# Kernel optimization log

Hardware: AMD Instinct MI355X
Metric: run time of the kernel (lower is better)

The kernel has to match this reference:

```python
import jax, jax.numpy as jnp
import numpy as np


def _dsconv(x, dw_w, dw_b, pw_w, pw_b):
    # depthwise 3x3 (padding=1, stride=1) + pointwise 1x1, both with bias (PyTorch Conv2d default)
    C = x.shape[1]
    y = jax.lax.conv_general_dilated(
        x, dw_w, window_strides=(1, 1), padding=((1, 1), (1, 1)),
        dimension_numbers=('NCHW', 'OIHW', 'NCHW'), feature_group_count=C)
    y = y + dw_b[None, :, None, None]
    y = jnp.einsum('bchw,oc->bohw', y, pw_w) + pw_b[None, :, None, None]
    return y


def setup_inputs() -> dict:
    key = jax.random.key(0)
    ks = jax.random.split(key, 16)
    B, C, H, W = 8, 256, 64, 256
    inp = {"x": jax.random.normal(ks[0], (B, C, H, W), dtype=jnp.float32)}
    chans = [(C, 128), (128, 64), (64, 32), (32, 9)]
    ki = 1
    for li, (ci, co) in enumerate(chans, start=1):
        inp[f"dw{li}_w"] = jax.random.normal(ks[ki], (ci, 1, 3, 3), dtype=jnp.float32) / 3.0; ki += 1
        inp[f"dw{li}_b"] = jnp.zeros((ci,), dtype=jnp.float32)
        inp[f"pw{li}_w"] = jax.random.normal(ks[ki], (co, ci), dtype=jnp.float32) / jnp.sqrt(jnp.float32(ci)); ki += 1
        inp[f"pw{li}_b"] = jnp.zeros((co,), dtype=jnp.float32)
    return inp


def reference(x,
              dw1_w, dw1_b, pw1_w, pw1_b,
              dw2_w, dw2_b, pw2_w, pw2_b,
              dw3_w, dw3_b, pw3_w, pw3_b,
              dw4_w, dw4_b, pw4_w, pw4_b):
    # la_conv stack: DSConv->ReLU x3, final DSConv (no relu), out channels = 9
    a = jax.nn.relu(_dsconv(x, dw1_w, dw1_b, pw1_w, pw1_b))
    a = jax.nn.relu(_dsconv(a, dw2_w, dw2_b, pw2_w, pw2_b))
    a = jax.nn.relu(_dsconv(a, dw3_w, dw3_b, pw3_w, pw3_b))
    a = _dsconv(a, dw4_w, dw4_b, pw4_w, pw4_b)            # (B,9,H,W)
    attn = jax.nn.softmax(a, axis=1)                      # softmax over the 9 taps

    B, C, H, W = x.shape
    xpad = jnp.pad(x, ((0, 0), (0, 0), (1, 1), (1, 1)))
    # dynamic 3x3 conv: out[b,c,i,j] = sum_{ki,kj} xpad[b,c,i+ki,j+kj] * attn[b,ki*3+kj,i,j]
    out = jnp.zeros_like(x)
    for ki in range(3):
        for kj in range(3):
            out = out + xpad[:, :, ki:ki + H, kj:kj + W] * attn[:, ki * 3 + kj][:, None, :, :]

    char_attn = attn.transpose(0, 2, 3, 1).reshape(B, H, W, 3, 3)
    return out, char_attn
```

## Files before the change

kernel.cpp:

```cpp
#include <hip/hip_runtime.h>
#include <math.h>

#define BH_ 64
#define BW_ 256
constexpr size_t HW = (size_t)BH_ * BW_;

using f32x4   = __attribute__((ext_vector_type(4))) float;
using short8  = __attribute__((ext_vector_type(8))) short;
using short4v = __attribute__((ext_vector_type(4))) short;

__device__ __forceinline__ short f2bf(float f) {
    unsigned u = __float_as_uint(f);
    u += 0x7fffu + ((u >> 16) & 1u);
    return (short)(u >> 16);
}
__device__ __forceinline__ float bf2f(short s) {
    return __uint_as_float(((unsigned)(unsigned short)s) << 16);
}

__device__ __forceinline__ int xcd_swizzle() {
    const int rb  = blockIdx.x;
    const int cpx = gridDim.x >> 3;
    return (rb & 7) * cpx + (rb >> 3);
}

__global__ __launch_bounds__(256)
void prep_kernel(const float* __restrict__ p1,
                 const float* __restrict__ p2,
                 const float* __restrict__ p3,
                 short* __restrict__ wb1,
                 short* __restrict__ wb2,
                 float* __restrict__ wt3)
{
    int idx = blockIdx.x * 256 + threadIdx.x;
    if (idx < 128 * 256) {
        wb1[idx] = f2bf(p1[idx]);
    } else if (idx < 128 * 256 + 64 * 128) {
        int r = idx - 128 * 256;
        wb2[r] = f2bf(p2[r]);
    } else if (idx < 128 * 256 + 64 * 128 + 32 * 64) {
        int r = idx - (128 * 256 + 64 * 128);
        int ci = r / 32, co = r % 32;
        wt3[r] = p3[co * 64 + ci];
    }
}

template<int CI, int CO, bool INBF>
__global__ __launch_bounds__(256, 4)
void dsconv_mfma(const void* __restrict__ xin_,
                 const float* __restrict__ dww,
                 const float* __restrict__ dwb,
                 const short* __restrict__ wBf,
                 const float* __restrict__ pwb,
                 short* __restrict__ out)
{
    constexpr int CIC = 32;
    constexpr int PX  = 64;
    constexpr int NT  = CO / 16;
    constexpr int WNT = NT / 4;
    constexpr int ST  = 40;
    constexpr int NC  = CI / CIC;
    static_assert(NT % 4 == 0 && CI % CIC == 0, "geometry");

    __shared__ short Abuf[2][PX * ST];

    const int t    = threadIdx.x;
    const int w    = t >> 6;
    const int lane = t & 63;
    const int bid  = xcd_swizzle();
    const int jt   = bid & 3;
    const int i    = (bid >> 2) & 63;
    const int b    = bid >> 8;
    const int j0   = jt * PX;

    const int ci_l = t >> 3;
    const int g    = t & 7;
    const int jq   = j0 + g * 8;
    const bool vtop = (i > 0), vbot = (i < BH_ - 1);

    const int lm = lane & 15;
    const int kb = lane >> 4;

    f32x4 acc[4][WNT];
    #pragma unroll
    for (int q = 0; q < WNT; ++q) {
        float bv = pwb[(w * WNT + q) * 16 + lm];
        #pragma unroll
        for (int mt = 0; mt < 4; ++mt) {
            f32x4 z = {bv, bv, bv, bv};
            acc[mt][q] = z;
        }
    }

    float  xw[3][10];
    float  wv9[9];
    float  dwbv;
    short8 bcur[WNT], bnxt[WNT];

    const short* bbase[WNT];
    #pragma unroll
    for (int q = 0; q < WNT; ++q)
        bbase[q] = wBf + (size_t)((w * WNT + q) * 16 + lm) * CI + kb * 8;

    auto LOADBF = [&](int cc, short8* dst) {
        #pragma unroll
        for (int q = 0; q < WNT; ++q)
            dst[q] = *reinterpret_cast<const short8*>(bbase[q] + cc);
    };

    auto LOADX = [&](int cc) {
        const int ci = cc + ci_l;
        #pragma unroll
        for (int di = 0; di < 3; ++di) {
            const bool ok = (di == 0) ? vtop : (di == 2) ? vbot : true;
            if (ok) {
                if constexpr (INBF) {
                    const short* xp = (const short*)xin_ + ((size_t)b * CI + ci) * HW;
                    const short* xr = xp + (size_t)(i + di - 1) * BW_ + jq;
                    xw[di][0] = (jq > 0) ? bf2f(xr[-1]) : 0.f;
                    short8 S = *reinterpret_cast<const short8*>(xr);
                    #pragma unroll
                    for (int e = 0; e < 8; ++e) xw[di][1 + e] = bf2f(S[e]);
                    xw[di][9] = (jq + 8 < BW_) ? bf2f(xr[8]) : 0.f;
                } else {
                    const float* xp = (const float*)xin_ + ((size_t)b * CI + ci) * HW;
                    const float* xr = xp + (size_t)(i + di - 1) * BW_ + jq;
                    xw[di][0] = (jq > 0) ? xr[-1] : 0.f;
                    float4 A = *reinterpret_cast<const float4*>(xr);
                    float4 Bq = *reinterpret_cast<const float4*>(xr + 4);
                    xw[di][1] = A.x; xw[di][2] = A.y; xw[di][3] = A.z; xw[di][4] = A.w;
                    xw[di][5] = Bq.x; xw[di][6] = Bq.y; xw[di][7] = Bq.z; xw[di][8] = Bq.w;
                    xw[di][9] = (jq + 8 < BW_) ? xr[8] : 0.f;
                }
            } else {
                #pragma unroll
                for (int e = 0; e < 10; ++e) xw[di][e] = 0.f;
            }
        }
        const float* wkp = dww + ci * 9;
        #pragma unroll
        for (int k = 0; k < 9; ++k) wv9[k] = wkp[k];
        dwbv = dwb[ci];
    };

    auto STOREA = [&](int nb) {
        float o[8];
        #pragma unroll
        for (int e = 0; e < 8; ++e) o[e] = dwbv;
        #pragma unroll
        for (int di = 0; di < 3; ++di) {
            const float w0 = wv9[di * 3 + 0];
            const float w1 = wv9[di * 3 + 1];
            const float w2 = wv9[di * 3 + 2];
            #pragma unroll
            for (int e = 0; e < 8; ++e)
                o[e] += w0 * xw[di][e] + w1 * xw[di][e + 1] + w2 * xw[di][e + 2];
        }
        #pragma unroll
        for (int e = 0; e < 8; ++e) {
            int px = g * 8 + e;
            int sa = (px * ST + ci_l) ^ (((px >> 3) & 7) << 3);
            Abuf[nb][sa] = f2bf(o[e]);
        }
    };

    auto MFMASTEP = [&](int nb) {
        #pragma unroll
        for (int mt = 0; mt < 4; ++mt) {
            int px = mt * 16 + lm;
            int sa = (px * ST + kb * 8) ^ (((px >> 3) & 7) << 3);
            short8 af = *reinterpret_cast<const short8*>(&Abuf[nb][sa]);
            #pragma unroll
            for (int q = 0; q < WNT; ++q)
                acc[mt][q] = __builtin_amdgcn_mfma_f32_16x16x32_bf16(
                    af, bcur[q], acc[mt][q], 0, 0, 0);
        }
    };

    LOADX(0); LOADBF(0, bcur);
    STOREA(0);
    __syncthreads();

    for (int c = 0; c < NC; ++c) {
        if (c + 1 < NC) { LOADX((c + 1) * CIC); LOADBF((c + 1) * CIC, bnxt); }
        MFMASTEP(c & 1);
        if (c + 1 < NC) {
            STOREA((c + 1) & 1);
            #pragma unroll
            for (int q = 0; q < WNT; ++q) bcur[q] = bnxt[q];
            __syncthreads();
        }
    }

    #pragma unroll
    for (int mt = 0; mt < 4; ++mt) {
        #pragma unroll
        for (int q = 0; q < WNT; ++q) {
            int co = (w * WNT + q) * 16 + lm;
            short* op = out + (((size_t)b * CO + co) * BH_ + i) * BW_
                        + j0 + mt * 16 + kb * 4;
            short4v v;
            v[0] = f2bf(fmaxf(acc[mt][q][0], 0.f));
            v[1] = f2bf(fmaxf(acc[mt][q][1], 0.f));
            v[2] = f2bf(fmaxf(acc[mt][q][2], 0.f));
            v[3] = f2bf(fmaxf(acc[mt][q][3], 0.f));
            *reinterpret_cast<short4v*>(op) = v;
        }
    }
}

template<int CI, int CO, int CPT>
__global__ __launch_bounds__(256, 4)
void dsconv_kernel(const short* __restrict__ xin,
                   const float* __restrict__ dww,
                   const float* __restrict__ dwb,
                   const float* __restrict__ wT,
                   const float* __restrict__ pwb,
                   short* __restrict__ out)
{
    constexpr int CIC = 32;
    constexpr int PX  = 64;
    static_assert(CO / CPT == 16, "co groups must be 16");

    __shared__ float dwbuf[CIC * PX];
    __shared__ float wbuf[CIC * CO];

    const int t   = threadIdx.x;
    const int bid = xcd_swizzle();
    const int jt  = bid & 3;
    const int i   = (bid >> 2) & 63;
    const int b   = bid >> 8;
    const int j0  = jt * PX;

    const int px_g = t & 15;
    const int co_g = t >> 4;
    const int co0  = co_g * CPT;
    const int p0   = px_g * 4;

    const int ci_local = t >> 3;
    const int g        = t & 7;
    const int jq       = j0 + g * 8;

    float acc[CPT][4];
    #pragma unroll
    for (int ii = 0; ii < CPT; ++ii) {
        float bv = pwb[co0 + ii];
        #pragma unroll
        for (int jj = 0; jj < 4; ++jj) acc[ii][jj] = bv;
    }

    for (int cc = 0; cc < CI; cc += CIC) {
        __syncthreads();
        {
            const float* src = wT + (size_t)cc * CO;
            #pragma unroll
            for (int idx = t * 4; idx < CIC * CO; idx += 1024)
                *reinterpret_cast<float4*>(&wbuf[idx]) =
                    *reinterpret_cast<const float4*>(&src[idx]);
        }
        {
            const int ci = cc + ci_local;
            const float* wk = dww + ci * 9;
            float w[9];
            #pragma unroll
            for (int k = 0; k < 9; ++k) w[k] = wk[k];
            float o[8];
            float bv = dwb[ci];
            #pragma unroll
            for (int e = 0; e < 8; ++e) o[e] = bv;

            const short* xp = xin + ((size_t)b * CI + ci) * HW;
            #pragma unroll
            for (int di = -1; di <= 1; ++di) {
                int ii2 = i + di;
                if ((unsigned)ii2 < (unsigned)BH_) {
                    const short* xr = xp + (size_t)ii2 * BW_ + jq;
                    float v[10];
                    v[0] = (jq > 0) ? bf2f(xr[-1]) : 0.f;
                    short8 S = *reinterpret_cast<const short8*>(xr);
                    #pragma unroll
                    for (int e = 0; e < 8; ++e) v[1 + e] = bf2f(S[e]);
                    v[9] = (jq + 8 < BW_) ? bf2f(xr[8]) : 0.f;
                    const float w0 = w[(di + 1) * 3 + 0];
                    const float w1 = w[(di + 1) * 3 + 1];
                    const float w2 = w[(di + 1) * 3 + 2];
                    #pragma unroll
                    for (int e = 0; e < 8; ++e)
                        o[e] += w0 * v[e] + w1 * v[e + 1] + w2 * v[e + 2];
                }
            }
            float4* dst = reinterpret_cast<float4*>(&dwbuf[ci_local * PX + g * 8]);
            dst[0] = make_float4(o[0], o[1], o[2], o[3]);
            dst[1] = make_float4(o[4], o[5], o[6], o[7]);
        }
        __syncthreads();

        #pragma unroll 4
        for (int k = 0; k < CIC; ++k) {
            float4 dq = *reinterpret_cast<const float4*>(&dwbuf[k * PX + p0]);
            float dv[4] = {dq.x, dq.y, dq.z, dq.w};
            float wv2[CPT];
            if constexpr (CPT == 2) {
                float2 wq = *reinterpret_cast<const float2*>(&wbuf[k * CO + co0]);
                wv2[0] = wq.x; wv2[1] = wq.y;
            } else {
                float4 wq = *reinterpret_cast<const float4*>(&wbuf[k * CO + co0]);
                #pragma unroll
                for (int ii = 0; ii < CPT && ii < 4; ++ii) wv2[ii] = (&wq.x)[ii];
            }
            #pragma unroll
            for (int ii = 0; ii < CPT; ++ii)
                #pragma unroll
                for (int jj = 0; jj < 4; ++jj)
                    acc[ii][jj] += wv2[ii] * dv[jj];
        }
    }

    #pragma unroll
    for (int ii = 0; ii < CPT; ++ii) {
        short4v v;
        v[0] = f2bf(fmaxf(acc[ii][0], 0.f));
        v[1] = f2bf(fmaxf(acc[ii][1], 0.f));
        v[2] = f2bf(fmaxf(acc[ii][2], 0.f));
        v[3] = f2bf(fmaxf(acc[ii][3], 0.f));
        short* op = out + (((size_t)b * CO + co0 + ii) * BH_ + i) * BW_ + j0 + p0;
        *reinterpret_cast<short4v*>(op) = v;
    }
}

__global__ __launch_bounds__(256, 4)
void final_kernel(const float* __restrict__ x,
                  const short* __restrict__ a3,
                  const float* __restrict__ dww,
                  const float* __restrict__ dwb,
                  const float* __restrict__ pww,
                  const float* __restrict__ pwb,
                  float* __restrict__ out,
                  float* __restrict__ chat)
{
    constexpr int PX = 64;
    __shared__ float dwbuf[32 * PX];
    __shared__ float attL[9][PX];

    const int t   = threadIdx.x;
    const int bid = xcd_swizzle();
    const int jt  = bid & 3;
    const int i   = (bid >> 2) & 63;
    const int b   = bid >> 8;
    const int j0  = jt * PX;
    const int g   = t & 7;
    const int jq  = j0 + g * 8;

    {
        const int ci = t >> 3;
        const float* wk = dww + ci * 9;
        float w[9];
        #pragma unroll
        for (int k = 0; k < 9; ++k) w[k] = wk[k];
        float o[8];
        float bv = dwb[ci];
        #pragma unroll
        for (int e = 0; e < 8; ++e) o[e] = bv;

        const short* xp = a3 + ((size_t)b * 32 + ci) * HW;
        #pragma unroll
        for (int di = -1; di <= 1; ++di) {
            int ii2 = i + di;
            if ((unsigned)ii2 < (unsigned)BH_) {
                const short* xr = xp + (size_t)ii2 * BW_ + jq;
                float v[10];
                v[0] = (jq > 0) ? bf2f(xr[-1]) : 0.f;
                short8 S = *reinterpret_cast<const short8*>(xr);
                #pragma unroll
                for (int e = 0; e < 8; ++e) v[1 + e] = bf2f(S[e]);
                v[9] = (jq + 8 < BW_) ? bf2f(xr[8]) : 0.f;
                const float w0 = w[(di + 1) * 3 + 0];
                const float w1 = w[(di + 1) * 3 + 1];
                const float w2 = w[(di + 1) * 3 + 2];
                #pragma unroll
                for (int e = 0; e < 8; ++e)
                    o[e] += w0 * v[e] + w1 * v[e + 1] + w2 * v[e + 2];
            }
        }
        float4* dst = reinterpret_cast<float4*>(&dwbuf[(t >> 3) * PX + g * 8]);
        dst[0] = make_float4(o[0], o[1], o[2], o[3]);
        dst[1] = make_float4(o[4], o[5], o[6], o[7]);
    }
    __syncthreads();

    for (int idx = t; idx < 9 * PX; idx += 256) {
        int co = idx >> 6;
        int px = idx & 63;
        float acc = pwb[co];
        #pragma unroll
        for (int ci = 0; ci < 32; ++ci)
            acc += pww[co * 32 + ci] * dwbuf[ci * PX + px];
        attL[co][px] = acc;
    }
    __syncthreads();

    if (t < PX) {
        float v[9];
        float m = -1e30f;
        #pragma unroll
        for (int k = 0; k < 9; ++k) { v[k] = attL[k][t]; m = fmaxf(m, v[k]); }
        float s = 0.f;
        #pragma unroll
        for (int k = 0; k < 9; ++k) { v[k] = __expf(v[k] - m); s += v[k]; }
        float inv = 1.f / s;
        #pragma unroll
        for (int k = 0; k < 9; ++k) attL[k][t] = v[k] * inv;
    }
    __syncthreads();

    {
        size_t base = (((size_t)b * BH_ + i) * BW_ + j0) * 9;
        for (int idx = t; idx < PX * 9; idx += 256)
            chat[base + idx] = attL[idx % 9][idx / 9];
    }

    float ar[9][8];
    #pragma unroll
    for (int k = 0; k < 9; ++k) {
        float4 a0 = *reinterpret_cast<const float4*>(&attL[k][g * 8]);
        float4 a1 = *reinterpret_cast<const float4*>(&attL[k][g * 8 + 4]);
        ar[k][0] = a0.x; ar[k][1] = a0.y; ar[k][2] = a0.z; ar[k][3] = a0.w;
        ar[k][4] = a1.x; ar[k][5] = a1.y; ar[k][6] = a1.z; ar[k][7] = a1.w;
    }

    const int c0 = t >> 3;
    for (int c = c0; c < 256; c += 32) {
        const float* xp = x + ((size_t)b * 256 + c) * HW;
        float v3[3][10];
        #pragma unroll
        for (int di = 0; di < 3; ++di) {
            int ii2 = i + di - 1;
            if ((unsigned)ii2 < (unsigned)BH_) {
                const float* xr = xp + (size_t)ii2 * BW_ + jq;
                v3[di][0] = (jq > 0) ? xr[-1] : 0.f;
                float4 A = *reinterpret_cast<const float4*>(xr);
                float4 Bq = *reinterpret_cast<const float4*>(xr + 4);
                v3[di][1] = A.x; v3[di][2] = A.y; v3[di][3] = A.z; v3[di][4] = A.w;
                v3[di][5] = Bq.x; v3[di][6] = Bq.y; v3[di][7] = Bq.z; v3[di][8] = Bq.w;
                v3[di][9] = (jq + 8 < BW_) ? xr[8] : 0.f;
            } else {
                #pragma unroll
                for (int e = 0; e < 10; ++e) v3[di][e] = 0.f;
            }
        }
        float o[8];
        #pragma unroll
        for (int e = 0; e < 8; ++e) o[e] = 0.f;
        #pragma unroll
        for (int di = 0; di < 3; ++di)
            #pragma unroll
            for (int dj = 0; dj < 3; ++dj)
                #pragma unroll
                for (int e = 0; e < 8; ++e)
                    o[e] += v3[di][e + dj] * ar[di * 3 + dj][e];
        float* op = out + ((size_t)b * 256 + c) * HW + (size_t)i * BW_ + jq;
        *reinterpret_cast<float4*>(op)     = make_float4(o[0], o[1], o[2], o[3]);
        *reinterpret_cast<float4*>(op + 4) = make_float4(o[4], o[5], o[6], o[7]);
    }
}

extern "C" void kernel_launch(void* const* d_in, const int* in_sizes, int n_in,
                              void* d_out, int out_size, void* d_ws, size_t ws_size,
                              hipStream_t stream)
{
    const float* x    = (const float*)d_in[0];
    const float* dw1w = (const float*)d_in[1];
    const float* dw1b = (const float*)d_in[2];
    const float* pw1w = (const float*)d_in[3];
    const float* pw1b = (const float*)d_in[4];
    const float* dw2w = (const float*)d_in[5];
    const float* dw2b = (const float*)d_in[6];
    const float* pw2w = (const float*)d_in[7];
    const float* pw2b = (const float*)d_in[8];
    const float* dw3w = (const float*)d_in[9];
    const float* dw3b = (const float*)d_in[10];
    const float* pw3w = (const float*)d_in[11];
    const float* pw3b = (const float*)d_in[12];
    const float* dw4w = (const float*)d_in[13];
    const float* dw4b = (const float*)d_in[14];
    const float* pw4w = (const float*)d_in[15];
    const float* pw4b = (const float*)d_in[16];

    float* outp = (float*)d_out;
    float* chat = outp + (size_t)8 * 256 * HW;

    short* wb1 = (short*)d_ws;
    short* wb2 = wb1 + 128 * 256;
    float* wt3 = (float*)((char*)d_ws + 81920);
    short* abase = (short*)((char*)d_ws + 90112);

    int kmax = 1;
    for (int k = 8; k >= 1; k >>= 1) {
        size_t need = 90112 + (size_t)k * (128 + 64) * HW * sizeof(short);
        if (need <= ws_size) { kmax = k; break; }
    }
    short* a1 = abase;
    short* a2 = a1 + (size_t)kmax * 128 * HW;
    short* a3 = a1;

    prep_kernel<<<(128 * 256 + 64 * 128 + 32 * 64 + 255) / 256, 256, 0, stream>>>(
        pw1w, pw2w, pw3w, wb1, wb2, wt3);

    for (int b0 = 0; b0 < 8; b0 += kmax) {
        int kc = (8 - b0 < kmax) ? (8 - b0) : kmax;
        const float* xb = x + (size_t)b0 * 256 * HW;
        int grid64 = kc * 256;

        dsconv_mfma<256, 128, false><<<grid64, 256, 0, stream>>>(
            xb, dw1w, dw1b, wb1, pw1b, a1);
        dsconv_mfma<128, 64, true><<<grid64, 256, 0, stream>>>(
            a1, dw2w, dw2b, wb2, pw2b, a2);
        dsconv_kernel<64, 32, 2><<<grid64, 256, 0, stream>>>(
            a2, dw3w, dw3b, wt3, pw3b, a3);
        final_kernel<<<grid64, 256, 0, stream>>>(
            xb, a3, dw4w, dw4b, pw4w, pw4b,
            outp + (size_t)b0 * 256 * HW, chat + (size_t)b0 * HW * 9);
    }
}
```

Before: 222.4 us.

## Stage full depthwise output in LDS once, then run MFMA loop without barriers

The double-buffered chunked pipeline is replaced by two phases. First every channel chunk's depthwise 3x3 result is computed and written into a single LDS tile holding all CI channels, followed by one barrier. Then the pointwise MFMA loop reads from that tile with no per-chunk __syncthreads. This removes a barrier per chunk and lets the compiler unroll freely, but LDS per block grows (for CI=256, about 33KB), which may cut occupancy, and depthwise global loads no longer overlap MFMA work.

```diff
diff --git a/kernel.cpp b/kernel.cpp
--- a/kernel.cpp
+++ b/kernel.cpp
@@ -58,11 +58,11 @@
     constexpr int PX  = 64;
     constexpr int NT  = CO / 16;
     constexpr int WNT = NT / 4;
-    constexpr int ST  = 40;
+    constexpr int ST  = CI + 8;
     constexpr int NC  = CI / CIC;
     static_assert(NT % 4 == 0 && CI % CIC == 0, "geometry");
 
-    __shared__ short Abuf[2][PX * ST];
+    __shared__ short Abuf[PX * ST];
 
     const int t    = threadIdx.x;
     const int w    = t >> 6;
@@ -81,6 +81,69 @@
     const int lm = lane & 15;
     const int kb = lane >> 4;
 
+    {
+        const int aswz = ((jq >> 3) & 7) << 3;
+        #pragma unroll
+        for (int c = 0; c < NC; ++c) {
+            const int cc = c * CIC;
+            const int ci = cc + ci_l;
+
+            float xw[3][10];
+            #pragma unroll
+            for (int di = 0; di < 3; ++di) {
+                const bool ok = (di == 0) ? vtop : (di == 2) ? vbot : true;
+                if (ok) {
+                    if constexpr (INBF) {
+                        const short* xp = (const short*)xin_ + ((size_t)b * CI + ci) * HW;
+                        const short* xr = xp + (size_t)(i + di - 1) * BW_ + jq;
+                        xw[di][0] = (jq > 0) ? bf2f(xr[-1]) : 0.f;
+                        short8 S = *reinterpret_cast<const short8*>(xr);
+                        #pragma unroll
+                        for (int e = 0; e < 8; ++e) xw[di][1 + e] = bf2f(S[e]);
+                        xw[di][9] = (jq + 8 < BW_) ? bf2f(xr[8]) : 0.f;
+                    } else {
+                        const float* xp = (const float*)xin_ + ((size_t)b * CI + ci) * HW;
+                        const float* xr = xp + (size_t)(i + di - 1) * BW_ + jq;
+                        xw[di][0] = (jq > 0) ? xr[-1] : 0.f;
+                        float4 A = *reinterpret_cast<const float4*>(xr);
+                        float4 Bq = *reinterpret_cast<const float4*>(xr + 4);
+                        xw[di][1] = A.x; xw[di][2] = A.y; xw[di][3] = A.z; xw[di][4] = A.w;
+                        xw[di][5] = Bq.x; xw[di][6] = Bq.y; xw[di][7] = Bq.z; xw[di][8] = Bq.w;
+                        xw[di][9] = (jq + 8 < BW_) ? xr[8] : 0.f;
+                    }
+                } else {
+                    #pragma unroll
+                    for (int e = 0; e < 10; ++e) xw[di][e] = 0.f;
+                }
+            }
+
+            const float* wkp = dww + ci * 9;
+            float o[8];
+            {
+                const float dwbv = dwb[ci];
+                #pragma unroll
+                for (int e = 0; e < 8; ++e) o[e] = dwbv;
+            }
+            #pragma unroll
+            for (int di = 0; di < 3; ++di) {
+                const float w0 = wkp[di * 3 + 0];
+                const float w1 = wkp[di * 3 + 1];
+                const float w2 = wkp[di * 3 + 2];
+                #pragma unroll
+                for (int e = 0; e < 8; ++e)
+                    o[e] += w0 * xw[di][e] + w1 * xw[di][e + 1] + w2 * xw[di][e + 2];
+            }
+            #pragma unroll
+            for (int e = 0; e < 8; ++e) {
+                int px = g * 8 + e;
+                int sa = (px * ST + ci) ^ aswz;
+                Abuf[sa] = f2bf(o[e]);
+            }
+        }
+    }
+
+    __syncthreads();
+
     f32x4 acc[4][WNT];
     #pragma unroll
     for (int q = 0; q < WNT; ++q) {
@@ -92,104 +155,35 @@
         }
     }
 
-    float  xw[3][10];
-    float  wv9[9];
-    float  dwbv;
-    short8 bcur[WNT], bnxt[WNT];
-
     const short* bbase[WNT];
     #pragma unroll
     for (int q = 0; q < WNT; ++q)
         bbase[q] = wBf + (size_t)((w * WNT + q) * 16 + lm) * CI + kb * 8;
 
-    auto LOADBF = [&](int cc, short8* dst) {
-        #pragma unroll
-        for (int q = 0; q < WNT; ++q)
-            dst[q] = *reinterpret_cast<const short8*>(bbase[q] + cc);
-    };
-
-    auto LOADX = [&](int cc) {
-        const int ci = cc + ci_l;
-        #pragma unroll
-        for (int di = 0; di < 3; ++di) {
-            const bool ok = (di == 0) ? vtop : (di == 2) ? vbot : true;
-            if (ok) {
-                if constexpr (INBF) {
-                    const short* xp = (const short*)xin_ + ((size_t)b * CI + ci) * HW;
-                    const short* xr = xp + (size_t)(i + di - 1) * BW_ + jq;
-                    xw[di][0] = (jq > 0) ? bf2f(xr[-1]) : 0.f;
-                    short8 S = *reinterpret_cast<const short8*>(xr);
-                    #pragma unroll
-                    for (int e = 0; e < 8; ++e) xw[di][1 + e] = bf2f(S[e]);
-                    xw[di][9] = (jq + 8 < BW_) ? bf2f(xr[8]) : 0.f;
-                } else {
-                    const float* xp = (const float*)xin_ + ((size_t)b * CI + ci) * HW;
-                    const float* xr = xp + (size_t)(i + di - 1) * BW_ + jq;
-                    xw[di][0] = (jq > 0) ? xr[-1] : 0.f;
-                    float4 A = *reinterpret_cast<const float4*>(xr);
-                    float4 Bq = *reinterpret_cast<const float4*>(xr + 4);
-                    xw[di][1] = A.x; xw[di][2] = A.y; xw[di][3] = A.z; xw[di][4] = A.w;
-                    xw[di][5] = Bq.x; xw[di][6] = Bq.y; xw[di][7] = Bq.z; xw[di][8] = Bq.w;
-                    xw[di][9] = (jq + 8 < BW_) ? xr[8] : 0.f;
-                }
-            } else {
-                #pragma unroll
-                for (int e = 0; e < 10; ++e) xw[di][e] = 0.f;
-            }
-        }
-        const float* wkp = dww + ci * 9;
-        #pragma unroll
-        for (int k = 0; k < 9; ++k) wv9[k] = wkp[k];
-        dwbv = dwb[ci];
-    };
-
-    auto STOREA = [&](int nb) {
-        float o[8];
-        #pragma unroll
-        for (int e = 0; e < 8; ++e) o[e] = dwbv;
-        #pragma unroll
-        for (int di = 0; di < 3; ++di) {
-            const float w0 = wv9[di * 3 + 0];
-            const float w1 = wv9[di * 3 + 1];
-            const float w2 = wv9[di * 3 + 2];
-            #pragma unroll
-            for (int e = 0; e < 8; ++e)
-                o[e] += w0 * xw[di][e] + w1 * xw[di][e + 1] + w2 * xw[di][e + 2];
-        }
-        #pragma unroll
-        for (int e = 0; e < 8; ++e) {
-            int px = g * 8 + e;
-            int sa = (px * ST + ci_l) ^ (((px >> 3) & 7) << 3);
-            Abuf[nb][sa] = f2bf(o[e]);
-        }
-    };
-
-    auto MFMASTEP = [&](int nb) {
+    short8 bcur[WNT], bnxt[WNT];
+    #pragma unroll
+    for (int q = 0; q < WNT; ++q)
+        bcur[q] = *reinterpret_cast<const short8*>(bbase[q]);
+
+    #pragma unroll
+    for (int c = 0; c < NC; ++c) {
+        if (c + 1 < NC) {
+            #pragma unroll
+            for (int q = 0; q < WNT; ++q)
+                bnxt[q] = *reinterpret_cast<const short8*>(bbase[q] + (c + 1) * CIC);
+        }
         #pragma unroll
         for (int mt = 0; mt < 4; ++mt) {
             int px = mt * 16 + lm;
-            int sa = (px * ST + kb * 8) ^ (((px >> 3) & 7) << 3);
-            short8 af = *reinterpret_cast<const short8*>(&Abuf[nb][sa]);
+            int sa = (px * ST + c * CIC + kb * 8) ^ (((px >> 3) & 7) << 3);
+            short8 af = *reinterpret_cast<const short8*>(&Abuf[sa]);
             #pragma unroll
             for (int q = 0; q < WNT; ++q)
                 acc[mt][q] = __builtin_amdgcn_mfma_f32_16x16x32_bf16(
                     af, bcur[q], acc[mt][q], 0, 0, 0);
         }
-    };
-
-    LOADX(0); LOADBF(0, bcur);
-    STOREA(0);
-    __syncthreads();
-
-    for (int c = 0; c < NC; ++c) {
-        if (c + 1 < NC) { LOADX((c + 1) * CIC); LOADBF((c + 1) * CIC, bnxt); }
-        MFMASTEP(c & 1);
-        if (c + 1 < NC) {
-            STOREA((c + 1) & 1);
-            #pragma unroll
-            for (int q = 0; q < WNT; ++q) bcur[q] = bnxt[q];
-            __syncthreads();
-        }
+        #pragma unroll
+        for (int q = 0; q < WNT; ++q) bcur[q] = bnxt[q];
     }
 
     #pragma unroll
```

Measured after the change: 220.6 us. Within noise of the previous version (-0.8%).

## Widen MFMA dsconv tiles to 128 pixels with 512 threads, waves split by pixel

Applied to the files above, without the earlier changes.

The first two depthwise-separable conv kernels now run 512-thread blocks that each cover 128 pixels of a row, halving the grid. Each wave now owns 16 pixels across all output channels, where before it owned 64 pixels and a slice of channels. Pointwise weights are read straight from global memory on every MFMA step, without register double-buffering. The aim is to reuse each depthwise input tile across more pixels and simplify the wave mapping. In exchange, weight-load latency is exposed inside the MFMA loop, and layer 1 now needs 32 accumulators per thread, which raises register pressure.

```diff
diff --git a/kernel.cpp b/kernel.cpp
--- a/kernel.cpp
+++ b/kernel.cpp
@@ -46,7 +46,7 @@
 }
 
 template<int CI, int CO, bool INBF>
-__global__ __launch_bounds__(256, 4)
+__global__ __launch_bounds__(512, 4)
 void dsconv_mfma(const void* __restrict__ xin_,
                  const float* __restrict__ dww,
                  const float* __restrict__ dwb,
@@ -55,12 +55,11 @@
                  short* __restrict__ out)
 {
     constexpr int CIC = 32;
-    constexpr int PX  = 64;
+    constexpr int PX  = 128;
     constexpr int NT  = CO / 16;
-    constexpr int WNT = NT / 4;
     constexpr int ST  = 40;
     constexpr int NC  = CI / CIC;
-    static_assert(NT % 4 == 0 && CI % CIC == 0, "geometry");
+    static_assert(CI % CIC == 0, "geometry");
 
     __shared__ short Abuf[2][PX * ST];
 
@@ -68,45 +67,30 @@
     const int w    = t >> 6;
     const int lane = t & 63;
     const int bid  = xcd_swizzle();
-    const int jt   = bid & 3;
-    const int i    = (bid >> 2) & 63;
-    const int b    = bid >> 8;
+    const int jt   = bid & 1;
+    const int i    = (bid >> 1) & 63;
+    const int b    = bid >> 7;
     const int j0   = jt * PX;
 
-    const int ci_l = t >> 3;
-    const int g    = t & 7;
+    const int ci_l = t >> 4;
+    const int g    = t & 15;
     const int jq   = j0 + g * 8;
     const bool vtop = (i > 0), vbot = (i < BH_ - 1);
 
     const int lm = lane & 15;
     const int kb = lane >> 4;
 
-    f32x4 acc[4][WNT];
+    f32x4 acc[NT];
     #pragma unroll
-    for (int q = 0; q < WNT; ++q) {
-        float bv = pwb[(w * WNT + q) * 16 + lm];
-        #pragma unroll
-        for (int mt = 0; mt < 4; ++mt) {
-            f32x4 z = {bv, bv, bv, bv};
-            acc[mt][q] = z;
-        }
-    }
-
-    float  xw[3][10];
-    float  wv9[9];
-    float  dwbv;
-    short8 bcur[WNT], bnxt[WNT];
-
-    const short* bbase[WNT];
-    #pragma unroll
-    for (int q = 0; q < WNT; ++q)
-        bbase[q] = wBf + (size_t)((w * WNT + q) * 16 + lm) * CI + kb * 8;
-
-    auto LOADBF = [&](int cc, short8* dst) {
-        #pragma unroll
-        for (int q = 0; q < WNT; ++q)
-            dst[q] = *reinterpret_cast<const short8*>(bbase[q] + cc);
-    };
+    for (int q = 0; q < NT; ++q) {
+        float bv = pwb[q * 16 + lm];
+        f32x4 z = {bv, bv, bv, bv};
+        acc[q] = z;
+    }
+
+    float xw[3][10];
+    float wv9[9];
+    float dwbv;
 
     auto LOADX = [&](int cc) {
         const int ci = cc + ci_l;
@@ -156,56 +140,51 @@
             for (int e = 0; e < 8; ++e)
                 o[e] += w0 * xw[di][e] + w1 * xw[di][e + 1] + w2 * xw[di][e + 2];
         }
+        const int aswz = (g & 7) << 3;
         #pragma unroll
         for (int e = 0; e < 8; ++e) {
             int px = g * 8 + e;
-            int sa = (px * ST + ci_l) ^ (((px >> 3) & 7) << 3);
+            int sa = (px * ST + ci_l) ^ aswz;
             Abuf[nb][sa] = f2bf(o[e]);
         }
     };
 
-    auto MFMASTEP = [&](int nb) {
-        #pragma unroll
-        for (int mt = 0; mt < 4; ++mt) {
-            int px = mt * 16 + lm;
-            int sa = (px * ST + kb * 8) ^ (((px >> 3) & 7) << 3);
-            short8 af = *reinterpret_cast<const short8*>(&Abuf[nb][sa]);
-            #pragma unroll
-            for (int q = 0; q < WNT; ++q)
-                acc[mt][q] = __builtin_amdgcn_mfma_f32_16x16x32_bf16(
-                    af, bcur[q], acc[mt][q], 0, 0, 0);
+    auto MFMASTEP = [&](int nb, int c) {
+        const int px = w * 16 + lm;
+        const int sa = (px * ST + kb * 8) ^ (((px >> 3) & 7) << 3);
+        short8 af = *reinterpret_cast<const short8*>(&Abuf[nb][sa]);
+        #pragma unroll
+        for (int q = 0; q < NT; ++q) {
+            short8 bf = *reinterpret_cast<const short8*>(
+                wBf + (size_t)(q * 16 + lm) * CI + c * CIC + kb * 8);
+            acc[q] = __builtin_amdgcn_mfma_f32_16x16x32_bf16(af, bf, acc[q], 0, 0, 0);
         }
     };
 
-    LOADX(0); LOADBF(0, bcur);
+    LOADX(0);
     STOREA(0);
     __syncthreads();
 
     for (int c = 0; c < NC; ++c) {
-        if (c + 1 < NC) { LOADX((c + 1) * CIC); LOADBF((c + 1) * CIC, bnxt); }
-        MFMASTEP(c & 1);
+        if (c + 1 < NC) LOADX((c + 1) * CIC);
+        MFMASTEP(c & 1, c);
         if (c + 1 < NC) {
             STOREA((c + 1) & 1);
-            #pragma unroll
-            for (int q = 0; q < WNT; ++q) bcur[q] = bnxt[q];
             __syncthreads();
         }
     }
 
     #pragma unroll
-    for (int mt = 0; mt < 4; ++mt) {
-        #pragma unroll
-        for (int q = 0; q < WNT; ++q) {
-            int co = (w * WNT + q) * 16 + lm;
-            short* op = out + (((size_t)b * CO + co) * BH_ + i) * BW_
-                        + j0 + mt * 16 + kb * 4;
-            short4v v;
-            v[0] = f2bf(fmaxf(acc[mt][q][0], 0.f));
-            v[1] = f2bf(fmaxf(acc[mt][q][1], 0.f));
-            v[2] = f2bf(fmaxf(acc[mt][q][2], 0.f));
-            v[3] = f2bf(fmaxf(acc[mt][q][3], 0.f));
-            *reinterpret_cast<short4v*>(op) = v;
-        }
+    for (int q = 0; q < NT; ++q) {
+        int co = q * 16 + lm;
+        short* op = out + (((size_t)b * CO + co) * BH_ + i) * BW_
+                    + j0 + w * 16 + kb * 4;
+        short4v v;
+        v[0] = f2bf(fmaxf(acc[q][0], 0.f));
+        v[1] = f2bf(fmaxf(acc[q][1], 0.f));
+        v[2] = f2bf(fmaxf(acc[q][2], 0.f));
+        v[3] = f2bf(fmaxf(acc[q][3], 0.f));
+        *reinterpret_cast<short4v*>(op) = v;
     }
 }
 
@@ -509,11 +488,12 @@
     for (int b0 = 0; b0 < 8; b0 += kmax) {
         int kc = (8 - b0 < kmax) ? (8 - b0) : kmax;
         const float* xb = x + (size_t)b0 * 256 * HW;
-        int grid64 = kc * 256;
-
-        dsconv_mfma<256, 128, false><<<grid64, 256, 0, stream>>>(
+        int grid128 = kc * 128;
+        int grid64  = kc * 256;
+
+        dsconv_mfma<256, 128, false><<<grid128, 512, 0, stream>>>(
             xb, dw1w, dw1b, wb1, pw1b, a1);
-        dsconv_mfma<128, 64, true><<<grid64, 256, 0, stream>>>(
+        dsconv_mfma<128, 64, true><<<grid128, 512, 0, stream>>>(
             a1, dw2w, dw2b, wb2, pw2b, a2);
         dsconv_kernel<64, 32, 2><<<grid64, 256, 0, stream>>>(
             a2, dw3w, dw3b, wt3, pw3b, a3);
```

Result: slower. 277.8 us (+24.9%).
